# Performance work log

Measured on AMD Instinct MI355X. Metric: run time of the kernel, lower is better.

Reference implementation:

```python
import jax, jax.numpy as jnp
import numpy as np

NEPOCHS = 100  # matches nepochs in init_kwargs


def lstm_cell(x, h, c, W_ih, W_hh, b_ih, b_hh):
    # PyTorch LSTM gate order: i, f, g, o
    gates = x @ W_ih.T + b_ih + h @ W_hh.T + b_hh  # (B, 4H)
    i, f, g, o = jnp.split(gates, 4, axis=-1)
    c_new = jax.nn.sigmoid(f) * c + jax.nn.sigmoid(i) * jnp.tanh(g)
    h_new = jax.nn.sigmoid(o) * jnp.tanh(c_new)
    return h_new, c_new


def setup_inputs() -> dict:
    key = jax.random.key(0)
    T, B, V, H, C = 400, 256, 128, 512, 64
    ks = jax.random.split(key, 8)
    s = 0.05
    return {
        "X": jax.random.normal(ks[0], (T, B, V), dtype=jnp.float32),
        "noise": jax.random.uniform(ks[1], (T, B, C), dtype=jnp.float32),
        "W_ih": jax.random.normal(ks[2], (4 * H, V + C), dtype=jnp.float32) * s,
        "W_hh": jax.random.normal(ks[3], (4 * H, H), dtype=jnp.float32) * s,
        "b_ih": jnp.zeros((4 * H,), jnp.float32),
        "b_hh": jnp.zeros((4 * H,), jnp.float32),
        "W_out": jax.random.normal(ks[4], (C, H), dtype=jnp.float32) * s,
        "b_out": jnp.zeros((C,), jnp.float32),
        "W_ctrl": jax.random.normal(ks[5], (C, H + C + 1), dtype=jnp.float32) * s,
        "b_ctrl": jnp.zeros((C,), jnp.float32),
        "epoch": 5,
    }


def reference(X, noise, W_ih, W_hh, b_ih, b_hh, W_out, b_out, W_ctrl, b_ctrl, epoch):
    T, B, V = X.shape
    C = W_out.shape[0]
    H = W_hh.shape[1]
    sg = jax.lax.stop_gradient
    # epsilon schedule: exp(-linspace(0, 7, nepochs))[epoch]  (training mode)
    eps = jnp.exp(-jnp.linspace(0.0, 7.0, NEPOCHS))[epoch]

    def step(carry, xs):
        h, c, y_bar, preds, halt_pts = carry
        x_t, n_t, t = xs
        # RNN input: raw features || detached halting indicators y_bar
        rnn_in = jnp.concatenate([x_t, sg(y_bar)], axis=-1)  # (B, V+C)
        h, c = lstm_cell(rnn_in, h, c, W_ih, W_hh, b_ih, b_hh)
        y_hat = jax.nn.sigmoid(h @ W_out.T + b_out)  # (B, C)
        time_col = t * jnp.ones((B, 1), X.dtype)
        # controller input is detached
        c_in = sg(jnp.concatenate([h, y_hat, time_col], axis=-1))  # (B, H+C+1)
        probs = jax.nn.sigmoid(c_in @ W_ctrl.T + b_ctrl)
        probs = (1.0 - eps) * probs + eps * 0.05  # explore/exploit smoothing
        a_t = n_t < probs  # Bernoulli sample via supplied uniform noise, (B,C) bool
        preds = jnp.where(a_t & (preds == 0.0), y_hat, preds)
        y_bar = jnp.where(a_t & (y_bar == 0.0), 1.0, y_bar)
        halt_pts = jnp.where((halt_pts == -1.0) & a_t, t, halt_pts)
        return (h, c, y_bar, preds, halt_pts), y_hat

    carry0 = (
        jnp.zeros((B, H), X.dtype),
        jnp.zeros((B, H), X.dtype),
        jnp.zeros((B, C), X.dtype),
        jnp.zeros((B, C), X.dtype),
        -jnp.ones((B, C), X.dtype),
    )
    ts = jnp.arange(T, dtype=X.dtype)
    (h, c, y_bar, preds, halt_pts), all_y = jax.lax.scan(step, carry0, (X, noise, ts))

    # classes never halted fall back to the last prediction
    y_hat_final = jnp.where(preds == 0.0, all_y[-1], preds)  # (B, C)
    halt_pts = jnp.where(halt_pts == -1.0, jnp.asarray(T - 1, X.dtype), halt_pts)
    mean_halting_point = (1.0 + sg(halt_pts)).mean() / (T + 1)
    return y_hat_final, mean_halting_point
```

## Files before the change

kernel.cpp:

```cpp
#include <hip/hip_runtime.h>
#include <math.h>

#define TT 400
#define BBATCH 256
#define VDIM 128
#define CDIM 64
#define HDIM 512
#define NCHUNK 11

typedef double d4 __attribute__((ext_vector_type(4)));

__device__ __forceinline__ double sigd(double x) {
  if (x >= 0.0) { double e = exp(-x); return 1.0 / (1.0 + e); }
  double e = exp(x); return e / (1.0 + e);
}

__global__ __launch_bounds__(256) void k_init(
    float* __restrict__ wtro, const float* __restrict__ W_out,
    float* __restrict__ wtrc, const float* __restrict__ W_ctrl,
    int* __restrict__ rowlive, int* __restrict__ alive)
{
  const int i = blockIdx.x * 256 + threadIdx.x;
  if (i < HDIM * CDIM) {
    const int k = i >> 6, c = i & 63;
    wtro[i] = W_out[c * HDIM + k];
  }
  if (i < 577 * CDIM) {
    const int k = i >> 6, c = i & 63;
    wtrc[i] = W_ctrl[c * 577 + k];
  }
  if (i < BBATCH) rowlive[i] = 1;
  if (i < TT) alive[i] = 0;
}

__global__ __launch_bounds__(256, 4) void k_phase1(
    const float* __restrict__ X, const float* __restrict__ W_ih,
    const float* __restrict__ W_hh, const float* __restrict__ b_ih,
    const float* __restrict__ b_hh, const double* __restrict__ hR,
    double* __restrict__ hW, double* __restrict__ cst,
    const double* __restrict__ ybar, const int* __restrict__ rowlive,
    const int* __restrict__ alive, int t)
{
  if (t > 0 && alive[t - 1] == 0) return;

  const int tid  = threadIdx.x;
  const int lane = tid & 63;
  const int wid  = tid >> 6;
  const int cb   = blockIdx.x;
  const int rb   = blockIdx.y;
  const int r0   = rb * 16;
  const int hbase = cb * 8;

  if (t > 0) {
    const unsigned long long m =
        __ballot((lane < 16) && (rowlive[r0 + (lane & 15)] != 0));
    if (m == 0ull) return;
  }

  __shared__ __align__(16) double aF[2][2][8][66];
  __shared__ __align__(16) float  bF[2][2][2][8][68];
  double* gsp = &aF[0][0][0][0];

  const int sA  = tid & 7;
  const int khA = (tid >> 3) & 1;
  const int rrA = tid >> 4;

  int rowm[4], colm[4];
  {
    d4 dp = {0.0, 0.0, 0.0, 0.0};
    const double ap = (lane < 16) ? (double)(lane + 1) : (lane < 32 ? 1.0 : 0.0);
    const double bp = (lane < 16) ? 1.0
                    : (lane < 32 ? 1000.0 * (double)((lane & 15) + 1) : 0.0);
    dp = __builtin_amdgcn_mfma_f64_16x16x4f64(ap, bp, dp, 0, 0, 0);
    #pragma unroll
    for (int r = 0; r < 4; ++r) {
      const int iv = (int)(dp[r] + 0.5);
      rowm[r] = ((iv % 1000) - 1) & 15;
      colm[r] = ((iv / 1000) - 1) & 15;
    }
  }

  double pa[4];
  float4 pw0, pw1;

  const int c0 = rrA, c1 = 16 + rrA;
  const int wg0 = (c0 >> 3) * HDIM + hbase + (c0 & 7);
  const int wg1 = (c1 >> 3) * HDIM + hbase + (c1 & 7);

  auto load_to = [&](int ci) {
    const int kk = ci * 64 + khA * 32 + sA * 4;
    const int rr = r0 + rrA;
    if (kk < VDIM) {
      const float4 v = *(const float4*)(X + ((size_t)t * BBATCH + rr) * VDIM + kk);
      pa[0] = v.x; pa[1] = v.y; pa[2] = v.z; pa[3] = v.w;
    } else if (t == 0) {
      pa[0] = 0.0; pa[1] = 0.0; pa[2] = 0.0; pa[3] = 0.0;
    } else if (kk < VDIM + CDIM) {
      const double2 v0 = *(const double2*)(ybar + (size_t)rr * CDIM + (kk - VDIM));
      const double2 v1 = *(const double2*)(ybar + (size_t)rr * CDIM + (kk - VDIM) + 2);
      pa[0] = v0.x; pa[1] = v0.y; pa[2] = v1.x; pa[3] = v1.y;
    } else {
      const double2 v0 = *(const double2*)(hR + (size_t)rr * HDIM + (kk - 192));
      const double2 v1 = *(const double2*)(hR + (size_t)rr * HDIM + (kk - 192) + 2);
      pa[0] = v0.x; pa[1] = v0.y; pa[2] = v1.x; pa[3] = v1.y;
    }
    pw0 = (kk < 192) ? *(const float4*)(W_ih + (size_t)wg0 * 192 + kk)
                     : *(const float4*)(W_hh + (size_t)wg0 * HDIM + (kk - 192));
    pw1 = (kk < 192) ? *(const float4*)(W_ih + (size_t)wg1 * 192 + kk)
                     : *(const float4*)(W_hh + (size_t)wg1 * HDIM + (kk - 192));
  };
  auto store_to = [&](int buf) {
    #pragma unroll
    for (int j = 0; j < 4; ++j)
      aF[buf][khA][sA][16 * j + rrA] = pa[j];
    *(float4*)&bF[buf][khA][0][sA][rrA * 4] = pw0;
    *(float4*)&bF[buf][khA][1][sA][rrA * 4] = pw1;
  };

  const int ct = wid & 1, kh = wid >> 1;
  d4 aa = {0.0, 0.0, 0.0, 0.0}, ab = aa;

  load_to(0);
  store_to(0);
  __syncthreads();

  for (int ci = 0; ci < NCHUNK; ++ci) {
    const int p = ci & 1;
    if (ci + 1 < NCHUNK) load_to(ci + 1);
    #pragma unroll
    for (int ss = 0; ss < 8; ++ss) {
      const double av = aF[p][kh][ss][lane];
      const double bv = (double)bF[p][kh][ct][ss][(lane & 15) * 4 + (lane >> 4)];
      if (ss & 1) ab = __builtin_amdgcn_mfma_f64_16x16x4f64(av, bv, ab, 0, 0, 0);
      else        aa = __builtin_amdgcn_mfma_f64_16x16x4f64(av, bv, aa, 0, 0, 0);
    }
    if (ci + 1 < NCHUNK) store_to(p ^ 1);
    __syncthreads();
  }
  const d4 acc = aa + ab;

  #pragma unroll
  for (int r = 0; r < 4; ++r)
    gsp[kh * 528 + rowm[r] * 33 + 16 * ct + colm[r]] = acc[r];
  __syncthreads();

  if (tid < 128) {
    const int jj = tid & 7, r = tid >> 3;
    const int g0 = hbase + jj;
    const double gi = gsp[r * 33 + jj]      + gsp[528 + r * 33 + jj]
                    + (double)b_ih[0 * HDIM + g0] + (double)b_hh[0 * HDIM + g0];
    const double gf = gsp[r * 33 + 8 + jj]  + gsp[528 + r * 33 + 8 + jj]
                    + (double)b_ih[1 * HDIM + g0] + (double)b_hh[1 * HDIM + g0];
    const double gg = gsp[r * 33 + 16 + jj] + gsp[528 + r * 33 + 16 + jj]
                    + (double)b_ih[2 * HDIM + g0] + (double)b_hh[2 * HDIM + g0];
    const double go = gsp[r * 33 + 24 + jj] + gsp[528 + r * 33 + 24 + jj]
                    + (double)b_ih[3 * HDIM + g0] + (double)b_hh[3 * HDIM + g0];
    const size_t oidx = (size_t)(r0 + r) * HDIM + g0;
    const double cold = (t == 0) ? 0.0 : cst[oidx];
    const double cn = sigd(gf) * cold + sigd(gi) * tanh(gg);
    const double hn = sigd(go) * tanh(cn);
    cst[oidx] = cn;
    hW[oidx]  = hn;
  }
}

__global__ __launch_bounds__(256) void k_phase2(
    const double* __restrict__ h, const float* __restrict__ wtro,
    const float* __restrict__ b_out, const float* __restrict__ wtrc,
    const float* __restrict__ b_ctrl, const float* __restrict__ noise,
    const int* __restrict__ epoch_p, double* __restrict__ ybar,
    double* __restrict__ preds, float* __restrict__ halt,
    double* __restrict__ ylast, int* __restrict__ rowlive,
    int* __restrict__ alive, int t)
{
  const int tid = threadIdx.x;
  const int b   = blockIdx.x;
  if (t > 0 && rowlive[b] == 0) return;

  __shared__ double hsh[HDIM];
  __shared__ double p1[4][64];
  __shared__ double p2[4][64];
  __shared__ double ysh[64];

  *(double2*)&hsh[2 * tid] = *(const double2*)(h + (size_t)b * HDIM + 2 * tid);
  __syncthreads();

  const int c = tid & 63, kq = tid >> 6;
  const int k0 = kq * 128;

  double s1 = 0.0, s2 = 0.0;
  #pragma unroll 8
  for (int k = k0; k < k0 + 128; ++k) {
    const double hk = hsh[k];
    s1 += hk * (double)wtro[k * 64 + c];
    s2 += hk * (double)wtrc[k * 64 + c];
  }
  p1[kq][c] = s1;
  p2[kq][c] = s2;
  __syncthreads();

  if (tid < 64)
    ysh[tid] = sigd(p1[0][tid] + p1[1][tid] + p1[2][tid] + p1[3][tid]
                    + (double)b_out[tid]);
  __syncthreads();

  if (tid < 64) {
    double a2 = p2[0][tid] + p2[1][tid] + p2[2][tid] + p2[3][tid];
    #pragma unroll 8
    for (int j = 0; j < CDIM; ++j)
      a2 += ysh[j] * (double)wtrc[(512 + j) * 64 + tid];
    a2 += (double)t * (double)wtrc[576 * 64 + tid] + (double)b_ctrl[tid];

    const double eps = exp(-7.0 * (double)(*epoch_p) / 99.0);
    const double pr  = (1.0 - eps) * sigd(a2) + eps * 0.05;
    const double n   = (double)noise[((size_t)t * BBATCH + b) * CDIM + tid];
    const bool   at  = n < pr;
    const double yh  = ysh[tid];
    const size_t i   = (size_t)b * CDIM + tid;

    const double pred_old = (t == 0) ? 0.0  : preds[i];
    const double ybar_old = (t == 0) ? 0.0  : ybar[i];
    const float  halt_old = (t == 0) ? -1.0f : halt[i];

    const double pred_new = (at && pred_old == 0.0) ? yh : pred_old;
    preds[i] = pred_new;
    ybar[i]  = (at && ybar_old == 0.0) ? 1.0 : ybar_old;
    halt[i]  = (halt_old == -1.0f && at) ? (float)t : halt_old;
    ylast[i] = yh;

    const unsigned long long m = __ballot(pred_new == 0.0);
    if (tid == 0) {
      rowlive[b] = (m != 0ull) ? 1 : 0;
      if (m != 0ull) atomicOr(alive + t, 1);
    }
  }
}

__global__ __launch_bounds__(256) void k_final_out(
    const double* __restrict__ preds, const double* __restrict__ ylast,
    float* __restrict__ out)
{
  const int i = blockIdx.x * 256 + threadIdx.x;
  const double p = preds[i];
  out[i] = (float)(p == 0.0 ? ylast[i] : p);
}

__global__ __launch_bounds__(256) void k_final_mean(
    const float* __restrict__ halt, float* __restrict__ out)
{
  __shared__ double s[256];
  double acc = 0.0;
  for (int i = threadIdx.x; i < BBATCH * CDIM; i += 256) {
    const float hp = halt[i];
    acc += 1.0 + (hp == -1.0f ? (double)(TT - 1) : (double)hp);
  }
  s[threadIdx.x] = acc;
  __syncthreads();
  for (int off = 128; off > 0; off >>= 1) {
    if (threadIdx.x < off) s[threadIdx.x] += s[threadIdx.x + off];
    __syncthreads();
  }
  if (threadIdx.x == 0)
    out[BBATCH * CDIM] = (float)(s[0] / (double)(BBATCH * CDIM) / (double)(TT + 1));
}

extern "C" void kernel_launch(void* const* d_in, const int* in_sizes, int n_in,
                              void* d_out, int out_size, void* d_ws, size_t ws_size,
                              hipStream_t stream)
{
  const float* X      = (const float*)d_in[0];
  const float* noise  = (const float*)d_in[1];
  const float* W_ih   = (const float*)d_in[2];
  const float* W_hh   = (const float*)d_in[3];
  const float* b_ih   = (const float*)d_in[4];
  const float* b_hh   = (const float*)d_in[5];
  const float* W_out  = (const float*)d_in[6];
  const float* b_out  = (const float*)d_in[7];
  const float* W_ctrl = (const float*)d_in[8];
  const float* b_ctrl = (const float*)d_in[9];
  const int*   epoch  = (const int*)d_in[10];
  float* out = (float*)d_out;

  char* ws = (char*)d_ws;
  double* h0      = (double*)ws;
  double* h1      = h0    + (size_t)BBATCH * HDIM;
  double* cst     = h1    + (size_t)BBATCH * HDIM;
  double* ybar    = cst   + (size_t)BBATCH * HDIM;
  double* preds   = ybar  + (size_t)BBATCH * CDIM;
  double* ylast   = preds + (size_t)BBATCH * CDIM;
  float*  halt    = (float*)(ylast + (size_t)BBATCH * CDIM);
  float*  wtro    = halt + (size_t)BBATCH * CDIM;
  float*  wtrc    = wtro + (size_t)HDIM * CDIM;
  int*    rowlive = (int*)(wtrc + (size_t)577 * CDIM);
  int*    alive   = rowlive + BBATCH;

  k_init<<<145, 256, 0, stream>>>(wtro, W_out, wtrc, W_ctrl, rowlive, alive);

  for (int t = 0; t < TT; ++t) {
    const double* hR = (t & 1) ? h1 : h0;
    double*       hW = (t & 1) ? h0 : h1;
    k_phase1<<<dim3(64, 16), 256, 0, stream>>>(X, W_ih, W_hh, b_ih, b_hh,
                                               hR, hW, cst, ybar, rowlive, alive, t);
    k_phase2<<<BBATCH, 256, 0, stream>>>(hW, wtro, b_out, wtrc, b_ctrl, noise,
                                         epoch, ybar, preds, halt, ylast,
                                         rowlive, alive, t);
  }

  k_final_out<<<64, 256, 0, stream>>>(preds, ylast, out);
  k_final_mean<<<1, 256, 0, stream>>>(halt, out);
}
```

Baseline: 4.211 ms.

## Fuse LSTM gate and controller phases into one launch per timestep

The two per-timestep kernels are merged into a single launch. The first 1024 blocks compute the LSTM gates and cell update. The last 256 blocks compute the output and controller work, and each one spin-waits on a per-row-block completion counter in global memory before reading the new hidden state. This halves the number of kernel launches across 400 serial steps and lets controller work for finished row blocks overlap with gate work still running on other row blocks. In exchange it relies on the spin-waiting blocks never starving the gate blocks of execution slots, and it adds atomics, fences and polling on every step.

```diff
diff --git a/kernel.cpp b/kernel.cpp
--- a/kernel.cpp
+++ b/kernel.cpp
@@ -7,6 +7,7 @@
 #define CDIM 64
 #define HDIM 512
 #define NCHUNK 11
+#define P1B 1024
 
 typedef double d4 __attribute__((ext_vector_type(4)));
 
@@ -18,7 +19,7 @@
 __global__ __launch_bounds__(256) void k_init(
     float* __restrict__ wtro, const float* __restrict__ W_out,
     float* __restrict__ wtrc, const float* __restrict__ W_ctrl,
-    int* __restrict__ rowlive, int* __restrict__ alive)
+    int* __restrict__ rowlive, int* __restrict__ alive, int* __restrict__ done)
 {
   const int i = blockIdx.x * 256 + threadIdx.x;
   if (i < HDIM * CDIM) {
@@ -31,207 +32,221 @@
   }
   if (i < BBATCH) rowlive[i] = 1;
   if (i < TT) alive[i] = 0;
-}
-
-__global__ __launch_bounds__(256, 4) void k_phase1(
+  if (i < TT * 16) done[i] = 0;
+}
+
+__global__ __launch_bounds__(256, 4) void k_step(
     const float* __restrict__ X, const float* __restrict__ W_ih,
     const float* __restrict__ W_hh, const float* __restrict__ b_ih,
-    const float* __restrict__ b_hh, const double* __restrict__ hR,
+    const float* __restrict__ b_hh, const float* __restrict__ wtro,
+    const float* __restrict__ b_out, const float* __restrict__ wtrc,
+    const float* __restrict__ b_ctrl, const float* __restrict__ noise,
+    const int* __restrict__ epoch_p, const double* __restrict__ hR,
     double* __restrict__ hW, double* __restrict__ cst,
-    const double* __restrict__ ybar, const int* __restrict__ rowlive,
-    const int* __restrict__ alive, int t)
-{
-  if (t > 0 && alive[t - 1] == 0) return;
-
+    double* __restrict__ ybar, double* __restrict__ preds,
+    float* __restrict__ halt, double* __restrict__ ylast,
+    int* __restrict__ rowlive, int* __restrict__ alive,
+    int* __restrict__ done, int t)
+{
   const int tid  = threadIdx.x;
   const int lane = tid & 63;
-  const int wid  = tid >> 6;
-  const int cb   = blockIdx.x;
-  const int rb   = blockIdx.y;
-  const int r0   = rb * 16;
-  const int hbase = cb * 8;
-
-  if (t > 0) {
-    const unsigned long long m =
-        __ballot((lane < 16) && (rowlive[r0 + (lane & 15)] != 0));
-    if (m == 0ull) return;
-  }
+  const int bid  = blockIdx.x;
+  if (t > 0 && alive[t - 1] == 0) return;
 
   __shared__ __align__(16) double aF[2][2][8][66];
   __shared__ __align__(16) float  bF[2][2][2][8][68];
-  double* gsp = &aF[0][0][0][0];
-
-  const int sA  = tid & 7;
-  const int khA = (tid >> 3) & 1;
-  const int rrA = tid >> 4;
-
-  int rowm[4], colm[4];
-  {
-    d4 dp = {0.0, 0.0, 0.0, 0.0};
-    const double ap = (lane < 16) ? (double)(lane + 1) : (lane < 32 ? 1.0 : 0.0);
-    const double bp = (lane < 16) ? 1.0
-                    : (lane < 32 ? 1000.0 * (double)((lane & 15) + 1) : 0.0);
-    dp = __builtin_amdgcn_mfma_f64_16x16x4f64(ap, bp, dp, 0, 0, 0);
+
+  if (bid < P1B) {
+    const int wid  = tid >> 6;
+    const int cb   = bid & 63;
+    const int rb   = bid >> 6;
+    const int r0   = rb * 16;
+    const int hbase = cb * 8;
+
+    if (t > 0) {
+      const unsigned long long m =
+          __ballot((lane < 16) && (rowlive[r0 + (lane & 15)] != 0));
+      if (m == 0ull) {
+        if (tid == 0) atomicAdd(&done[t * 16 + rb], 1);
+        return;
+      }
+    }
+
+    double* gsp = &aF[0][0][0][0];
+
+    const int sA  = tid & 7;
+    const int khA = (tid >> 3) & 1;
+    const int rrA = tid >> 4;
+
+    int rowm[4], colm[4];
+    {
+      d4 dp = {0.0, 0.0, 0.0, 0.0};
+      const double ap = (lane < 16) ? (double)(lane + 1) : (lane < 32 ? 1.0 : 0.0);
+      const double bp = (lane < 16) ? 1.0
+                      : (lane < 32 ? 1000.0 * (double)((lane & 15) + 1) : 0.0);
+      dp = __builtin_amdgcn_mfma_f64_16x16x4f64(ap, bp, dp, 0, 0, 0);
+      #pragma unroll
+      for (int r = 0; r < 4; ++r) {
+        const int iv = (int)(dp[r] + 0.5);
+        rowm[r] = ((iv % 1000) - 1) & 15;
+        colm[r] = ((iv / 1000) - 1) & 15;
+      }
+    }
+
+    double pa[4];
+    float4 pw0, pw1;
+    const int c0 = rrA, c1 = 16 + rrA;
+    const int wg0 = (c0 >> 3) * HDIM + hbase + (c0 & 7);
+    const int wg1 = (c1 >> 3) * HDIM + hbase + (c1 & 7);
+
+    auto load_to = [&](int ci) {
+      const int kk = ci * 64 + khA * 32 + sA * 4;
+      const int rr = r0 + rrA;
+      if (kk < VDIM) {
+        const float4 v = *(const float4*)(X + ((size_t)t * BBATCH + rr) * VDIM + kk);
+        pa[0] = v.x; pa[1] = v.y; pa[2] = v.z; pa[3] = v.w;
+      } else if (t == 0) {
+        pa[0] = 0.0; pa[1] = 0.0; pa[2] = 0.0; pa[3] = 0.0;
+      } else if (kk < VDIM + CDIM) {
+        const double2 v0 = *(const double2*)(ybar + (size_t)rr * CDIM + (kk - VDIM));
+        const double2 v1 = *(const double2*)(ybar + (size_t)rr * CDIM + (kk - VDIM) + 2);
+        pa[0] = v0.x; pa[1] = v0.y; pa[2] = v1.x; pa[3] = v1.y;
+      } else {
+        const double2 v0 = *(const double2*)(hR + (size_t)rr * HDIM + (kk - 192));
+        const double2 v1 = *(const double2*)(hR + (size_t)rr * HDIM + (kk - 192) + 2);
+        pa[0] = v0.x; pa[1] = v0.y; pa[2] = v1.x; pa[3] = v1.y;
+      }
+      pw0 = (kk < 192) ? *(const float4*)(W_ih + (size_t)wg0 * 192 + kk)
+                       : *(const float4*)(W_hh + (size_t)wg0 * HDIM + (kk - 192));
+      pw1 = (kk < 192) ? *(const float4*)(W_ih + (size_t)wg1 * 192 + kk)
+                       : *(const float4*)(W_hh + (size_t)wg1 * HDIM + (kk - 192));
+    };
+    auto store_to = [&](int buf) {
+      #pragma unroll
+      for (int j = 0; j < 4; ++j)
+        aF[buf][khA][sA][16 * j + rrA] = pa[j];
+      *(float4*)&bF[buf][khA][0][sA][rrA * 4] = pw0;
+      *(float4*)&bF[buf][khA][1][sA][rrA * 4] = pw1;
+    };
+
+    const int ct = tid >> 6 & 1, kh = wid >> 1;
+    d4 aa = {0.0, 0.0, 0.0, 0.0}, ab = aa;
+
+    load_to(0);
+    store_to(0);
+    __syncthreads();
+
+    for (int ci = 0; ci < NCHUNK; ++ci) {
+      const int p = ci & 1;
+      if (ci + 1 < NCHUNK) load_to(ci + 1);
+      #pragma unroll
+      for (int ss = 0; ss < 8; ++ss) {
+        const double av = aF[p][kh][ss][lane];
+        const double bv = (double)bF[p][kh][ct][ss][(lane & 15) * 4 + (lane >> 4)];
+        if (ss & 1) ab = __builtin_amdgcn_mfma_f64_16x16x4f64(av, bv, ab, 0, 0, 0);
+        else        aa = __builtin_amdgcn_mfma_f64_16x16x4f64(av, bv, aa, 0, 0, 0);
+      }
+      if (ci + 1 < NCHUNK) store_to(p ^ 1);
+      __syncthreads();
+    }
+    const d4 acc = aa + ab;
+
     #pragma unroll
-    for (int r = 0; r < 4; ++r) {
-      const int iv = (int)(dp[r] + 0.5);
-      rowm[r] = ((iv % 1000) - 1) & 15;
-      colm[r] = ((iv / 1000) - 1) & 15;
-    }
-  }
-
-  double pa[4];
-  float4 pw0, pw1;
-
-  const int c0 = rrA, c1 = 16 + rrA;
-  const int wg0 = (c0 >> 3) * HDIM + hbase + (c0 & 7);
-  const int wg1 = (c1 >> 3) * HDIM + hbase + (c1 & 7);
-
-  auto load_to = [&](int ci) {
-    const int kk = ci * 64 + khA * 32 + sA * 4;
-    const int rr = r0 + rrA;
-    if (kk < VDIM) {
-      const float4 v = *(const float4*)(X + ((size_t)t * BBATCH + rr) * VDIM + kk);
-      pa[0] = v.x; pa[1] = v.y; pa[2] = v.z; pa[3] = v.w;
-    } else if (t == 0) {
-      pa[0] = 0.0; pa[1] = 0.0; pa[2] = 0.0; pa[3] = 0.0;
-    } else if (kk < VDIM + CDIM) {
-      const double2 v0 = *(const double2*)(ybar + (size_t)rr * CDIM + (kk - VDIM));
-      const double2 v1 = *(const double2*)(ybar + (size_t)rr * CDIM + (kk - VDIM) + 2);
-      pa[0] = v0.x; pa[1] = v0.y; pa[2] = v1.x; pa[3] = v1.y;
-    } else {
-      const double2 v0 = *(const double2*)(hR + (size_t)rr * HDIM + (kk - 192));
-      const double2 v1 = *(const double2*)(hR + (size_t)rr * HDIM + (kk - 192) + 2);
-      pa[0] = v0.x; pa[1] = v0.y; pa[2] = v1.x; pa[3] = v1.y;
-    }
-    pw0 = (kk < 192) ? *(const float4*)(W_ih + (size_t)wg0 * 192 + kk)
-                     : *(const float4*)(W_hh + (size_t)wg0 * HDIM + (kk - 192));
-    pw1 = (kk < 192) ? *(const float4*)(W_ih + (size_t)wg1 * 192 + kk)
-                     : *(const float4*)(W_hh + (size_t)wg1 * HDIM + (kk - 192));
-  };
-  auto store_to = [&](int buf) {
-    #pragma unroll
-    for (int j = 0; j < 4; ++j)
-      aF[buf][khA][sA][16 * j + rrA] = pa[j];
-    *(float4*)&bF[buf][khA][0][sA][rrA * 4] = pw0;
-    *(float4*)&bF[buf][khA][1][sA][rrA * 4] = pw1;
-  };
-
-  const int ct = wid & 1, kh = wid >> 1;
-  d4 aa = {0.0, 0.0, 0.0, 0.0}, ab = aa;
-
-  load_to(0);
-  store_to(0);
-  __syncthreads();
-
-  for (int ci = 0; ci < NCHUNK; ++ci) {
-    const int p = ci & 1;
-    if (ci + 1 < NCHUNK) load_to(ci + 1);
-    #pragma unroll
-    for (int ss = 0; ss < 8; ++ss) {
-      const double av = aF[p][kh][ss][lane];
-      const double bv = (double)bF[p][kh][ct][ss][(lane & 15) * 4 + (lane >> 4)];
-      if (ss & 1) ab = __builtin_amdgcn_mfma_f64_16x16x4f64(av, bv, ab, 0, 0, 0);
-      else        aa = __builtin_amdgcn_mfma_f64_16x16x4f64(av, bv, aa, 0, 0, 0);
-    }
-    if (ci + 1 < NCHUNK) store_to(p ^ 1);
-    __syncthreads();
-  }
-  const d4 acc = aa + ab;
-
-  #pragma unroll
-  for (int r = 0; r < 4; ++r)
-    gsp[kh * 528 + rowm[r] * 33 + 16 * ct + colm[r]] = acc[r];
-  __syncthreads();
-
-  if (tid < 128) {
-    const int jj = tid & 7, r = tid >> 3;
-    const int g0 = hbase + jj;
-    const double gi = gsp[r * 33 + jj]      + gsp[528 + r * 33 + jj]
-                    + (double)b_ih[0 * HDIM + g0] + (double)b_hh[0 * HDIM + g0];
-    const double gf = gsp[r * 33 + 8 + jj]  + gsp[528 + r * 33 + 8 + jj]
-                    + (double)b_ih[1 * HDIM + g0] + (double)b_hh[1 * HDIM + g0];
-    const double gg = gsp[r * 33 + 16 + jj] + gsp[528 + r * 33 + 16 + jj]
-                    + (double)b_ih[2 * HDIM + g0] + (double)b_hh[2 * HDIM + g0];
-    const double go = gsp[r * 33 + 24 + jj] + gsp[528 + r * 33 + 24 + jj]
-                    + (double)b_ih[3 * HDIM + g0] + (double)b_hh[3 * HDIM + g0];
-    const size_t oidx = (size_t)(r0 + r) * HDIM + g0;
-    const double cold = (t == 0) ? 0.0 : cst[oidx];
-    const double cn = sigd(gf) * cold + sigd(gi) * tanh(gg);
-    const double hn = sigd(go) * tanh(cn);
-    cst[oidx] = cn;
-    hW[oidx]  = hn;
-  }
-}
-
-__global__ __launch_bounds__(256) void k_phase2(
-    const double* __restrict__ h, const float* __restrict__ wtro,
-    const float* __restrict__ b_out, const float* __restrict__ wtrc,
-    const float* __restrict__ b_ctrl, const float* __restrict__ noise,
-    const int* __restrict__ epoch_p, double* __restrict__ ybar,
-    double* __restrict__ preds, float* __restrict__ halt,
-    double* __restrict__ ylast, int* __restrict__ rowlive,
-    int* __restrict__ alive, int t)
-{
-  const int tid = threadIdx.x;
-  const int b   = blockIdx.x;
-  if (t > 0 && rowlive[b] == 0) return;
-
-  __shared__ double hsh[HDIM];
-  __shared__ double p1[4][64];
-  __shared__ double p2[4][64];
-  __shared__ double ysh[64];
-
-  *(double2*)&hsh[2 * tid] = *(const double2*)(h + (size_t)b * HDIM + 2 * tid);
-  __syncthreads();
-
-  const int c = tid & 63, kq = tid >> 6;
-  const int k0 = kq * 128;
-
-  double s1 = 0.0, s2 = 0.0;
-  #pragma unroll 8
-  for (int k = k0; k < k0 + 128; ++k) {
-    const double hk = hsh[k];
-    s1 += hk * (double)wtro[k * 64 + c];
-    s2 += hk * (double)wtrc[k * 64 + c];
-  }
-  p1[kq][c] = s1;
-  p2[kq][c] = s2;
-  __syncthreads();
-
-  if (tid < 64)
-    ysh[tid] = sigd(p1[0][tid] + p1[1][tid] + p1[2][tid] + p1[3][tid]
-                    + (double)b_out[tid]);
-  __syncthreads();
-
-  if (tid < 64) {
-    double a2 = p2[0][tid] + p2[1][tid] + p2[2][tid] + p2[3][tid];
+    for (int r = 0; r < 4; ++r)
+      gsp[kh * 528 + rowm[r] * 33 + 16 * ct + colm[r]] = acc[r];
+    __syncthreads();
+
+    if (tid < 128) {
+      const int jj = tid & 7, r = tid >> 3;
+      const int g0 = hbase + jj;
+      const double gi = gsp[r * 33 + jj]      + gsp[528 + r * 33 + jj]
+                      + (double)b_ih[0 * HDIM + g0] + (double)b_hh[0 * HDIM + g0];
+      const double gf = gsp[r * 33 + 8 + jj]  + gsp[528 + r * 33 + 8 + jj]
+                      + (double)b_ih[1 * HDIM + g0] + (double)b_hh[1 * HDIM + g0];
+      const double gg = gsp[r * 33 + 16 + jj] + gsp[528 + r * 33 + 16 + jj]
+                      + (double)b_ih[2 * HDIM + g0] + (double)b_hh[2 * HDIM + g0];
+      const double go = gsp[r * 33 + 24 + jj] + gsp[528 + r * 33 + 24 + jj]
+                      + (double)b_ih[3 * HDIM + g0] + (double)b_hh[3 * HDIM + g0];
+      const size_t oidx = (size_t)(r0 + r) * HDIM + g0;
+      const double cold = (t == 0) ? 0.0 : cst[oidx];
+      const double cn = sigd(gf) * cold + sigd(gi) * tanh(gg);
+      const double hn = sigd(go) * tanh(cn);
+      cst[oidx] = cn;
+      hW[oidx]  = hn;
+    }
+
+    __syncthreads();
+    if (tid == 0) {
+      __threadfence();
+      atomicAdd(&done[t * 16 + rb], 1);
+    }
+  } else {
+    const int b = bid - P1B;
+    if (t > 0 && rowlive[b] == 0) return;
+
+    if (tid == 0) {
+      while (atomicAdd(&done[t * 16 + (b >> 4)], 0) < 64)
+        __builtin_amdgcn_s_sleep(2);
+      __threadfence();
+    }
+    __syncthreads();
+
+    double* hsh = &aF[0][0][0][0];
+    double* p1  = hsh + HDIM;
+    double* p2  = p1 + 256;
+    double* ysh = p2 + 256;
+
+    *(double2*)&hsh[2 * tid] = *(const double2*)(hW + (size_t)b * HDIM + 2 * tid);
+    __syncthreads();
+
+    const int c = tid & 63, kq = tid >> 6;
+    const int k0 = kq * 128;
+
+    double s1 = 0.0, s2 = 0.0;
     #pragma unroll 8
-    for (int j = 0; j < CDIM; ++j)
-      a2 += ysh[j] * (double)wtrc[(512 + j) * 64 + tid];
-    a2 += (double)t * (double)wtrc[576 * 64 + tid] + (double)b_ctrl[tid];
-
-    const double eps = exp(-7.0 * (double)(*epoch_p) / 99.0);
-    const double pr  = (1.0 - eps) * sigd(a2) + eps * 0.05;
-    const double n   = (double)noise[((size_t)t * BBATCH + b) * CDIM + tid];
-    const bool   at  = n < pr;
-    const double yh  = ysh[tid];
-    const size_t i   = (size_t)b * CDIM + tid;
-
-    const double pred_old = (t == 0) ? 0.0  : preds[i];
-    const double ybar_old = (t == 0) ? 0.0  : ybar[i];
-    const float  halt_old = (t == 0) ? -1.0f : halt[i];
-
-    const double pred_new = (at && pred_old == 0.0) ? yh : pred_old;
-    preds[i] = pred_new;
-    ybar[i]  = (at && ybar_old == 0.0) ? 1.0 : ybar_old;
-    halt[i]  = (halt_old == -1.0f && at) ? (float)t : halt_old;
-    ylast[i] = yh;
-
-    const unsigned long long m = __ballot(pred_new == 0.0);
-    if (tid == 0) {
-      rowlive[b] = (m != 0ull) ? 1 : 0;
-      if (m != 0ull) atomicOr(alive + t, 1);
+    for (int k = k0; k < k0 + 128; ++k) {
+      const double hk = hsh[k];
+      s1 += hk * (double)wtro[k * 64 + c];
+      s2 += hk * (double)wtrc[k * 64 + c];
+    }
+    p1[kq * 64 + c] = s1;
+    p2[kq * 64 + c] = s2;
+    __syncthreads();
+
+    if (tid < 64)
+      ysh[tid] = sigd(p1[tid] + p1[64 + tid] + p1[128 + tid] + p1[192 + tid]
+                      + (double)b_out[tid]);
+    __syncthreads();
+
+    if (tid < 64) {
+      double a2 = p2[tid] + p2[64 + tid] + p2[128 + tid] + p2[192 + tid];
+      #pragma unroll 8
+      for (int j = 0; j < CDIM; ++j)
+        a2 += ysh[j] * (double)wtrc[(512 + j) * 64 + tid];
+      a2 += (double)t * (double)wtrc[576 * 64 + tid] + (double)b_ctrl[tid];
+
+      const double eps = exp(-7.0 * (double)(*epoch_p) / 99.0);
+      const double pr  = (1.0 - eps) * sigd(a2) + eps * 0.05;
+      const double n   = (double)noise[((size_t)t * BBATCH + b) * CDIM + tid];
+      const bool   at  = n < pr;
+      const double yh  = ysh[tid];
+      const size_t i   = (size_t)b * CDIM + tid;
+
+      const double pred_old = (t == 0) ? 0.0  : preds[i];
+      const double ybar_old = (t == 0) ? 0.0  : ybar[i];
+      const float  halt_old = (t == 0) ? -1.0f : halt[i];
+
+      const double pred_new = (at && pred_old == 0.0) ? yh : pred_old;
+      preds[i] = pred_new;
+      ybar[i]  = (at && ybar_old == 0.0) ? 1.0 : ybar_old;
+      halt[i]  = (halt_old == -1.0f && at) ? (float)t : halt_old;
+      ylast[i] = yh;
+
+      const unsigned long long m = __ballot(pred_new == 0.0);
+      if (tid == 0) {
+        rowlive[b] = (m != 0ull) ? 1 : 0;
+        if (m != 0ull) atomicOr(alive + t, 1);
+      }
     }
   }
 }
@@ -293,17 +308,16 @@
   float*  wtrc    = wtro + (size_t)HDIM * CDIM;
   int*    rowlive = (int*)(wtrc + (size_t)577 * CDIM);
   int*    alive   = rowlive + BBATCH;
-
-  k_init<<<145, 256, 0, stream>>>(wtro, W_out, wtrc, W_ctrl, rowlive, alive);
+  int*    done    = alive + TT;
+
+  k_init<<<145, 256, 0, stream>>>(wtro, W_out, wtrc, W_ctrl, rowlive, alive, done);
 
   for (int t = 0; t < TT; ++t) {
     const double* hR = (t & 1) ? h1 : h0;
     double*       hW = (t & 1) ? h0 : h1;
-    k_phase1<<<dim3(64, 16), 256, 0, stream>>>(X, W_ih, W_hh, b_ih, b_hh,
-                                               hR, hW, cst, ybar, rowlive, alive, t);
-    k_phase2<<<BBATCH, 256, 0, stream>>>(hW, wtro, b_out, wtrc, b_ctrl, noise,
-                                         epoch, ybar, preds, halt, ylast,
-                                         rowlive, alive, t);
+    k_step<<<P1B + BBATCH, 256, 0, stream>>>(
+        X, W_ih, W_hh, b_ih, b_hh, wtro, b_out, wtrc, b_ctrl, noise, epoch,
+        hR, hW, cst, ybar, preds, halt, ylast, rowlive, alive, done, t);
   }
 
   k_final_out<<<64, 256, 0, stream>>>(preds, ylast, out);
```

Result: slower. 7.979 ms (+89.5%).
